# Optimization experiments

Hardware: AMD Instinct MI355X
Metric: run time of the kernel (lower is better)

## Reference

```python
import jax, jax.numpy as jnp
import numpy as np

M_BLOCK = 8  # N:M group size along in_features

def nm_mask(shape, m):
    """Deterministic VENOM mask from VenomSparsifier.get_random_mask:
    keep positions 0 and 2 in every m-sized group along the last dim."""
    pat = np.zeros(m, dtype=np.float32)
    pat[0] = 1.0
    pat[2] = 1.0
    mask = np.tile(pat, shape[-1] // m)  # [in_features]
    return jnp.asarray(np.broadcast_to(mask, shape))

def setup_inputs() -> dict:
    key = jax.random.key(0)
    k1, k2, k3 = jax.random.split(key, 3)
    B, S, D_IN, D_OUT = 4, 4096, 4096, 4096
    x = jax.random.normal(k1, (B, S, D_IN), dtype=jnp.float32)
    weight = jax.random.normal(k2, (D_OUT, D_IN), dtype=jnp.float32) * 0.02
    bias = jax.random.normal(k3, (D_OUT,), dtype=jnp.float32) * 0.02
    return {"x": x, "weight": weight, "bias": bias}

def reference(x, weight, bias):
    # Structured-sparse linear: y = x @ (W * mask).T + b
    w_sp = weight * nm_mask(weight.shape, M_BLOCK)  # [out, in], 2:8 sparse
    out = jnp.einsum('bsk,nk->bsn', x, w_sp) + bias  # [B, S, out]
    return out
```

## Files before the change

### kernel.cpp

```cpp
#include <hip/hip_runtime.h>
#include <hip/hip_bf16.h>
#include <stdint.h>


typedef __attribute__((ext_vector_type(8))) short short8;
typedef __attribute__((ext_vector_type(4))) float float4_t;

typedef unsigned short u16;
typedef unsigned int   u32;

#define M_TOT 16384
#define N_TOT 4096
#define K_ACT 4096
#define K_C   1024

typedef __attribute__((address_space(1))) void GlobVoid;
typedef __attribute__((address_space(3))) void LdsVoid;

static __device__ __forceinline__ u32 f32_to_bf16_rne(float f) {
    u32 u = __float_as_uint(f);
    u32 rounded = u + 0x7FFFu + ((u >> 16) & 1u);
    return rounded >> 16;
}

__global__ __launch_bounds__(256) void compact_k(const float4* __restrict__ src,
                                                 u32* __restrict__ dst, int n) {
    int i = blockIdx.x * 256 + threadIdx.x;
    if (i >= n) return;
    float4 g = src[(size_t)i * 2];
    dst[i] = f32_to_bf16_rne(g.x) | (f32_to_bf16_rne(g.z) << 16);
}

__global__ __launch_bounds__(256) void gemm_bt(const u16* __restrict__ A,
                                               const u16* __restrict__ B,
                                               const float* __restrict__ bias,
                                               float* __restrict__ C) {
    __shared__ u16 Als[128 * 32];
    __shared__ u16 Bls[128 * 32];

    const int tid  = threadIdx.x;
    const int lane = tid & 63;
    const int wave = tid >> 6;
    const int m0   = blockIdx.y * 128;
    const int n0   = blockIdx.x * 128;

    const int wm = (wave & 1) * 64;
    const int wn = (wave >> 1) * 64;
    const int fr = lane & 15;
    const int kq = (lane >> 4) * 8;

    const int srow = lane >> 2;
    const int scol = (lane & 3) * 8;

    float4_t acc[4][4];
    const float4_t fzero = {0.f, 0.f, 0.f, 0.f};
#pragma unroll
    for (int i = 0; i < 4; ++i)
#pragma unroll
        for (int j = 0; j < 4; ++j) acc[i][j] = fzero;

    for (int kt = 0; kt < K_C; kt += 32) {
        __syncthreads();
#pragma unroll
        for (int c = 0; c < 2; ++c) {
            const int ch  = wave * 2 + c;
            const int row = ch * 16 + srow;
            const u16* ga = A + (size_t)(m0 + row) * K_C + kt + scol;
            __builtin_amdgcn_global_load_lds((GlobVoid*)ga, (LdsVoid*)&Als[ch * 512],
                                             16, 0, 0);
            const u16* gb = B + (size_t)(n0 + row) * K_C + kt + scol;
            __builtin_amdgcn_global_load_lds((GlobVoid*)gb, (LdsVoid*)&Bls[ch * 512],
                                             16, 0, 0);
        }
        __syncthreads();

        short8 af[4], bf[4];
#pragma unroll
        for (int i = 0; i < 4; ++i)
            af[i] = *(const short8*)&Als[(wm + i * 16 + fr) * 32 + kq];
#pragma unroll
        for (int j = 0; j < 4; ++j)
            bf[j] = *(const short8*)&Bls[(wn + j * 16 + fr) * 32 + kq];

#pragma unroll
        for (int i = 0; i < 4; ++i)
#pragma unroll
            for (int j = 0; j < 4; ++j)
                acc[i][j] = __builtin_amdgcn_mfma_f32_16x16x32_bf16(
                    af[i], bf[j], acc[i][j], 0, 0, 0);
    }

    const int rbase = m0 + wm + (lane >> 4) * 4;
    const int cbase = n0 + wn + fr;
#pragma unroll
    for (int j = 0; j < 4; ++j) {
        const int col  = cbase + j * 16;
        const float bj = bias[col];
#pragma unroll
        for (int i = 0; i < 4; ++i) {
            const int row = rbase + i * 16;
#pragma unroll
            for (int r = 0; r < 4; ++r) {
                C[(size_t)(row + r) * N_TOT + col] = acc[i][j][r] + bj;
            }
        }
    }
}

__global__ __launch_bounds__(256) void fallback_k(const float* __restrict__ X,
                                                  const float* __restrict__ W,
                                                  const float* __restrict__ bias,
                                                  float* __restrict__ out) {
    size_t idx = (size_t)blockIdx.x * 256 + threadIdx.x;
    int n    = (int)(idx & (N_TOT - 1));
    size_t m = idx >> 12;
    const float* xr = X + m * K_ACT;
    const float* wr = W + (size_t)n * K_ACT;
    float acc = 0.f;
    for (int g = 0; g < K_ACT / 8; ++g) {
        acc += xr[g * 8] * wr[g * 8] + xr[g * 8 + 2] * wr[g * 8 + 2];
    }
    out[idx] = acc + bias[n];
}

extern "C" void kernel_launch(void* const* d_in, const int* in_sizes, int n_in,
                              void* d_out, int out_size, void* d_ws, size_t ws_size,
                              hipStream_t stream) {
    const float* x    = (const float*)d_in[0];
    const float* w    = (const float*)d_in[1];
    const float* bias = (const float*)d_in[2];
    float* out = (float*)d_out;

    const size_t xc_elems = (size_t)M_TOT * K_C;
    const size_t wc_elems = (size_t)N_TOT * K_C;
    const size_t need = (xc_elems + wc_elems) * sizeof(u16);

    if (ws_size >= need) {
        u16* xc = (u16*)d_ws;
        u16* wc = xc + xc_elems;

        const int ngx = M_TOT * (K_ACT / 8);
        const int ngw = N_TOT * (K_ACT / 8);
        compact_k<<<ngx / 256, 256, 0, stream>>>((const float4*)x, (u32*)xc, ngx);
        compact_k<<<ngw / 256, 256, 0, stream>>>((const float4*)w, (u32*)wc, ngw);

        dim3 grid(N_TOT / 128, M_TOT / 128);
        gemm_bt<<<grid, 256, 0, stream>>>(xc, wc, bias, out);
    } else {
        const size_t total = (size_t)M_TOT * N_TOT;
        fallback_k<<<(int)(total / 256), 256, 0, stream>>>(x, w, bias, out);
    }
}
```

Before: 638.7 us.

## Rewrite sparse GEMM as 256x256 tile, 8-wave, double-buffered pipelined kernel

Replaces the 128x128 single-buffered GEMM with a 256x256 tile per 512-thread workgroup. K-step 64 tiles are staged in LDS in half-tile quarters with double buffering, global-to-LDS loads are interleaved with MFMA phases, and waits use explicit vmcnt/lgkmcnt and barriers. It also adds an XOR swizzle on LDS columns to reduce bank conflicts, a workgroup index swizzle for L2 locality, and setprio around the MFMA blocks. The aim is to hide load latency and raise arithmetic intensity. The cost is 128KB of LDS per workgroup and fragile hand-scheduled synchronisation.

```diff
diff --git a/kernel.cpp b/kernel.cpp
--- a/kernel.cpp
+++ b/kernel.cpp
@@ -1,5 +1,4 @@
 #include <hip/hip_runtime.h>
-#include <hip/hip_bf16.h>
 #include <stdint.h>
 
 
@@ -13,6 +12,7 @@
 #define N_TOT 4096
 #define K_ACT 4096
 #define K_C   1024
+#define NT    16
 
 typedef __attribute__((address_space(1))) void GlobVoid;
 typedef __attribute__((address_space(3))) void LdsVoid;
@@ -31,77 +31,146 @@
     dst[i] = f32_to_bf16_rne(g.x) | (f32_to_bf16_rne(g.z) << 16);
 }
 
-__global__ __launch_bounds__(256) void gemm_bt(const u16* __restrict__ A,
-                                               const u16* __restrict__ B,
-                                               const float* __restrict__ bias,
-                                               float* __restrict__ C) {
-    __shared__ u16 Als[128 * 32];
-    __shared__ u16 Bls[128 * 32];
+static __device__ __forceinline__ void stage_half(const u16* __restrict__ src,
+                                                  int row0, int kt,
+                                                  u16* lds_half,
+                                                  int wave, int lane) {
+#pragma unroll
+    for (int c = 0; c < 2; ++c) {
+        const int blk = c * 8 + wave;
+        const int r   = blk * 8 + (lane >> 3);
+        const int cb  = (lane & 7) * 16;
+        const int cbs = cb ^ ((r & 4) << 3);
+        const u16* g = src + (size_t)(row0 + r) * K_C + kt * 64 + (cbs >> 1);
+        __builtin_amdgcn_global_load_lds((GlobVoid*)g,
+                                         (LdsVoid*)(lds_half + blk * 512),
+                                         16, 0, 0);
+    }
+}
+
+
+#define PHASE(ABASE, BBASE, MH, NH, STAGE_STMT, VMCNT_STMT)                     \
+    do {                                                                        \
+        short8 afr[4][2], bfr[2][2];                                            \
+        const u16* Ah = lds + (ABASE);                                          \
+        const u16* Bh = lds + (BBASE);                                          \
+        _Pragma("unroll")                                                       \
+        for (int i = 0; i < 4; ++i) {                                           \
+            afr[i][0] = *(const short8*)(Ah + arow + i * 1024 + ck0);           \
+            afr[i][1] = *(const short8*)(Ah + arow + i * 1024 + ck1);           \
+        }                                                                       \
+        _Pragma("unroll")                                                       \
+        for (int j = 0; j < 2; ++j) {                                           \
+            bfr[j][0] = *(const short8*)(Bh + brow + j * 1024 + ck0);           \
+            bfr[j][1] = *(const short8*)(Bh + brow + j * 1024 + ck1);           \
+        }                                                                       \
+        STAGE_STMT;                                                             \
+        __builtin_amdgcn_s_barrier();                                           \
+        asm volatile("s_waitcnt lgkmcnt(0)" ::: "memory");                      \
+        __builtin_amdgcn_sched_barrier(0);                                      \
+        __builtin_amdgcn_s_setprio(1);                                          \
+        _Pragma("unroll")                                                       \
+        for (int i = 0; i < 4; ++i) {                                           \
+            _Pragma("unroll")                                                   \
+            for (int j = 0; j < 2; ++j) {                                       \
+                acc[MH][NH][i][j] = __builtin_amdgcn_mfma_f32_16x16x32_bf16(    \
+                    afr[i][0], bfr[j][0], acc[MH][NH][i][j], 0, 0, 0);          \
+                acc[MH][NH][i][j] = __builtin_amdgcn_mfma_f32_16x16x32_bf16(    \
+                    afr[i][1], bfr[j][1], acc[MH][NH][i][j], 0, 0, 0);          \
+            }                                                                   \
+        }                                                                       \
+        __builtin_amdgcn_s_setprio(0);                                          \
+        VMCNT_STMT;                                                             \
+        __builtin_amdgcn_s_barrier();                                           \
+    } while (0)
+
+__global__ __launch_bounds__(512, 2) void gemm_bt(const u16* __restrict__ A,
+                                                  const u16* __restrict__ B,
+                                                  const float* __restrict__ bias,
+                                                  float* __restrict__ C) {
+    __shared__ u16 lds[65536];
 
     const int tid  = threadIdx.x;
     const int lane = tid & 63;
     const int wave = tid >> 6;
-    const int m0   = blockIdx.y * 128;
-    const int n0   = blockIdx.x * 128;
-
-    const int wm = (wave & 1) * 64;
-    const int wn = (wave >> 1) * 64;
-    const int fr = lane & 15;
-    const int kq = (lane >> 4) * 8;
-
-    const int srow = lane >> 2;
-    const int scol = (lane & 3) * 8;
-
-    float4_t acc[4][4];
+    const int wm   = wave >> 2;
+    const int wn   = wave & 3;
+    const int fr   = lane & 15;
+    const int q    = lane >> 4;
+
+    const int wg  = blockIdx.x;
+    const int swz = (wg & 7) * 128 + (wg >> 3);
+    const int m0  = (swz >> 4) * 256;
+    const int n0  = (swz & 15) * 256;
+
+    const int ck0 = (((0 * 64) + q * 16) ^ ((fr & 4) << 3)) >> 1;
+    const int ck1 = (((1 * 64) + q * 16) ^ ((fr & 4) << 3)) >> 1;
+    const int arow = (wm * 64 + fr) * 64;
+    const int brow = (wn * 32 + fr) * 64;
+
+    float4_t acc[2][2][4][2];
     const float4_t fzero = {0.f, 0.f, 0.f, 0.f};
 #pragma unroll
-    for (int i = 0; i < 4; ++i)
-#pragma unroll
-        for (int j = 0; j < 4; ++j) acc[i][j] = fzero;
-
-    for (int kt = 0; kt < K_C; kt += 32) {
-        __syncthreads();
-#pragma unroll
-        for (int c = 0; c < 2; ++c) {
-            const int ch  = wave * 2 + c;
-            const int row = ch * 16 + srow;
-            const u16* ga = A + (size_t)(m0 + row) * K_C + kt + scol;
-            __builtin_amdgcn_global_load_lds((GlobVoid*)ga, (LdsVoid*)&Als[ch * 512],
-                                             16, 0, 0);
-            const u16* gb = B + (size_t)(n0 + row) * K_C + kt + scol;
-            __builtin_amdgcn_global_load_lds((GlobVoid*)gb, (LdsVoid*)&Bls[ch * 512],
-                                             16, 0, 0);
-        }
-        __syncthreads();
-
-        short8 af[4], bf[4];
-#pragma unroll
-        for (int i = 0; i < 4; ++i)
-            af[i] = *(const short8*)&Als[(wm + i * 16 + fr) * 32 + kq];
-#pragma unroll
-        for (int j = 0; j < 4; ++j)
-            bf[j] = *(const short8*)&Bls[(wn + j * 16 + fr) * 32 + kq];
-
-#pragma unroll
-        for (int i = 0; i < 4; ++i)
-#pragma unroll
-            for (int j = 0; j < 4; ++j)
-                acc[i][j] = __builtin_amdgcn_mfma_f32_16x16x32_bf16(
-                    af[i], bf[j], acc[i][j], 0, 0, 0);
-    }
-
-    const int rbase = m0 + wm + (lane >> 4) * 4;
-    const int cbase = n0 + wn + fr;
-#pragma unroll
-    for (int j = 0; j < 4; ++j) {
-        const int col  = cbase + j * 16;
-        const float bj = bias[col];
-#pragma unroll
-        for (int i = 0; i < 4; ++i) {
-            const int row = rbase + i * 16;
-#pragma unroll
-            for (int r = 0; r < 4; ++r) {
-                C[(size_t)(row + r) * N_TOT + col] = acc[i][j][r] + bj;
+    for (int mh = 0; mh < 2; ++mh)
+#pragma unroll
+        for (int nh = 0; nh < 2; ++nh)
+#pragma unroll
+            for (int i = 0; i < 4; ++i)
+#pragma unroll
+                for (int j = 0; j < 2; ++j) acc[mh][nh][i][j] = fzero;
+
+    stage_half(A, m0 + 0,   0, lds + 0,     wave, lane);
+    stage_half(B, n0 + 0,   0, lds + 16384, wave, lane);
+    stage_half(A, m0 + 128, 0, lds + 8192,  wave, lane);
+    stage_half(B, n0 + 128, 0, lds + 24576, wave, lane);
+    stage_half(A, m0 + 0,   1, lds + 32768, wave, lane);
+    stage_half(B, n0 + 0,   1, lds + 49152, wave, lane);
+    asm volatile("s_waitcnt vmcnt(4)" ::: "memory");
+    __builtin_amdgcn_s_barrier();
+
+    for (int it = 0; it < NT / 2; ++it) {
+        const int u  = 2 * it;
+        const int t1 = u + 1;
+        const int t2 = (u + 2 < NT) ? u + 2 : NT - 1;
+        const int t3 = (u + 3 < NT) ? u + 3 : NT - 1;
+
+        PHASE(0, 16384, 0, 0,
+              stage_half(A, m0 + 128, t1, lds + 40960, wave, lane), ((void)0));
+        PHASE(0, 24576, 0, 1,
+              stage_half(B, n0 + 128, t1, lds + 57344, wave, lane), ((void)0));
+        PHASE(8192, 16384, 1, 0,
+              stage_half(A, m0 + 0, t2, lds + 0, wave, lane), ((void)0));
+        PHASE(8192, 24576, 1, 1,
+              stage_half(B, n0 + 0, t2, lds + 16384, wave, lane),
+              asm volatile("s_waitcnt vmcnt(4)" ::: "memory"));
+        PHASE(32768, 49152, 0, 0,
+              stage_half(A, m0 + 128, t2, lds + 8192, wave, lane), ((void)0));
+        PHASE(32768, 57344, 0, 1,
+              stage_half(B, n0 + 128, t2, lds + 24576, wave, lane), ((void)0));
+        PHASE(40960, 49152, 1, 0,
+              stage_half(A, m0 + 0, t3, lds + 32768, wave, lane), ((void)0));
+        PHASE(40960, 57344, 1, 1,
+              stage_half(B, n0 + 0, t3, lds + 49152, wave, lane),
+              asm volatile("s_waitcnt vmcnt(4)" ::: "memory"));
+    }
+
+    const int rq = (lane >> 4) * 4;
+#pragma unroll
+    for (int nh = 0; nh < 2; ++nh) {
+#pragma unroll
+        for (int j = 0; j < 2; ++j) {
+            const int col  = n0 + nh * 128 + wn * 32 + j * 16 + fr;
+            const float bj = bias[col];
+#pragma unroll
+            for (int mh = 0; mh < 2; ++mh) {
+#pragma unroll
+                for (int i = 0; i < 4; ++i) {
+                    const int row = m0 + mh * 128 + wm * 64 + i * 16 + rq;
+#pragma unroll
+                    for (int r = 0; r < 4; ++r) {
+                        C[(size_t)(row + r) * N_TOT + col] = acc[mh][nh][i][j][r] + bj;
+                    }
+                }
             }
         }
     }
@@ -144,8 +213,7 @@
         compact_k<<<ngx / 256, 256, 0, stream>>>((const float4*)x, (u32*)xc, ngx);
         compact_k<<<ngw / 256, 256, 0, stream>>>((const float4*)w, (u32*)wc, ngw);
 
-        dim3 grid(N_TOT / 128, M_TOT / 128);
-        gemm_bt<<<grid, 256, 0, stream>>>(xc, wc, bias, out);
+        gemm_bt<<<dim3(1024), dim3(512), 0, stream>>>(xc, wc, bias, out);
     } else {
         const size_t total = (size_t)M_TOT * N_TOT;
         fallback_k<<<(int)(total / 256), 256, 0, stream>>>(x, w, bias, out);
```

After: 639.2 us. No clear change (+0.1%).
